# Kernel optimization log

Hardware: AMD Instinct MI355X
Metric: run time of the kernel (lower is better)

The kernel has to match this reference:

```python
import jax, jax.numpy as jnp
import numpy as np

K = 64        # num_clusters
S1 = 5        # num_shadow + 1
C = 128       # dim
ALPHA = 1500.0
EPS = 1e-12


def setup_inputs() -> dict:
    key = jax.random.key(0)
    k1, k2 = jax.random.split(key)
    x = jax.random.normal(k1, (8, C, 44, 44), dtype=jnp.float32)
    centroids = jax.random.normal(k2, (K, S1, C), dtype=jnp.float32) * 0.01
    return {"x": x, "centroids": centroids}


def reference(x, centroids):
    N = x.shape[0]
    # conv params derived from centroids, as in _init_params
    w = (2.0 * ALPHA) * centroids.reshape(K * S1, C)            # (K*S1, C)
    b = -ALPHA * jnp.linalg.norm(centroids.reshape(K * S1, C), axis=1)  # (K*S1,)

    xf = x.reshape(N, C, -1)                                    # (N, C, P)
    # 1x1 conv == GEMM over channel dim
    logits = jnp.einsum('mc,ncp->nmp', w, xf) + b[None, :, None]
    logits = logits.reshape(N, K, S1, -1)                       # (N, K, S1, P)

    soft_alpha = jax.nn.softmax(logits[:, :, 0:1, :], axis=1)   # (N, K, 1, P)
    soft_beta = jax.nn.softmax(logits, axis=2)[:, :, 0:1, :]    # (N, K, 1, P)
    soft_assign = soft_alpha * soft_beta                        # (N, K, 1, P)

    # residual = x - rep_centroid; then residual *= (1 + soft_assign); sum over P.
    # sum_p (x[n,c,p] - rep[k,c]) * w[n,k,p]
    #   = einsum(w, x) - rep[k,c] * sum_p w[n,k,p]   (same math, no (N,K,C,P) tensor)
    w_assign = 1.0 + soft_assign[:, :, 0, :]                    # (N, K, P)
    rep = centroids[:, 0, :]                                    # (K, C)
    out = jnp.einsum('nkp,ncp->nkc', w_assign, xf) \
          - rep[None, :, :] * jnp.sum(w_assign, axis=-1)[:, :, None]  # (N, K, C)

    # intra-cluster L2 normalize (dim=2), flatten, global L2 normalize
    out = out / jnp.maximum(jnp.linalg.norm(out, axis=2, keepdims=True), EPS)
    flat = out.reshape(N, -1)
    flat = flat / jnp.maximum(jnp.linalg.norm(flat, axis=1, keepdims=True), EPS)
    return (flat, soft_assign)
```

## Files before the change

kernel.cpp:

```cpp
#include <hip/hip_runtime.h>
#include <math.h>

#define NB 8
#define KC 64
#define S1C 5
#define CC 128
#define PP 1936
#define PT 64
#define NPT 31
#define NTILE (NB * NPT)
#define ALPHAF 1500.0f
#define EPSF 1e-12f

#define WS_PART  ((size_t)NTILE * KC * CC)
#define WS_MAIN_FLOATS (WS_PART + (size_t)NTILE * KC)

typedef __attribute__((ext_vector_type(8))) short short8;
typedef __attribute__((ext_vector_type(4))) float f32x4;

__device__ __forceinline__ void split8(const float4 a, const float4 b,
                                       short8& h, short8& l) {
    const float f[8] = {a.x, a.y, a.z, a.w, b.x, b.y, b.z, b.w};
#pragma unroll
    for (int j = 0; j < 8; ++j) {
        const unsigned u  = __float_as_uint(f[j]);
        const unsigned hi = u & 0xffff0000u;
        const float lo    = f[j] - __uint_as_float(hi);
        h[j] = (short)(hi >> 16);
        l[j] = (short)(__float_as_uint(lo) >> 16);
    }
}

__global__ __launch_bounds__(1024, 4) void k1_main(
    const float* __restrict__ x, const float* __restrict__ cen,
    float* __restrict__ sa_out, float* __restrict__ outC,
    float* __restrict__ outS, int mode)
{
    __shared__ __align__(16) unsigned short xh [64 * 128];
    __shared__ __align__(16) unsigned short xl [64 * 128];
    __shared__ __align__(16) unsigned short xch[128 * 64];
    __shared__ __align__(16) unsigned short xcl[128 * 64];
    __shared__ __align__(16) unsigned short wah[64 * 64];
    __shared__ __align__(16) unsigned short wal[64 * 64];
    __shared__ float2 ap[16 * 66];

    const int tid  = threadIdx.x;
    const int lane = tid & 63;
    const int wid  = tid >> 6;
    const int quad = lane >> 4;
    const int l15  = lane & 15;
    const int bx   = blockIdx.x;
    const int n    = bx / NPT;
    const int pt   = bx - n * NPT;
    const int p0   = pt * PT;

    int wrow[2]; bool wvalid[2];
#pragma unroll
    for (int i = 0; i < 2; ++i) {
        const int mp = (2 * wid + i) * 16 + l15;
        const int s  = mp & 7;
        wvalid[i] = (s < 5);
        wrow[i]   = 5 * (mp >> 3) + s;
    }

    float4 pv0[2], pv1[2];
#pragma unroll
    for (int i = 0; i < 2; ++i) {
        pv0[i] = make_float4(0.f, 0.f, 0.f, 0.f);
        pv1[i] = pv0[i];
        if (wvalid[i]) {
            const float* wp = cen + (size_t)wrow[i] * CC + quad * 8;
            pv0[i] = *(const float4*)wp;
            pv1[i] = *(const float4*)(wp + 4);
        }
    }

    const float* xn = x + (size_t)n * CC * PP;
    {
        const int pl = tid & 63;
        const int c0 = (tid >> 6) * 8;
        const bool pv = (p0 + pl) < PP;
        const float* src = xn + p0 + pl;
        float v[8];
#pragma unroll
        for (int i = 0; i < 8; ++i)
            v[i] = pv ? src[(size_t)(c0 + i) * PP] : 0.f;
        unsigned short hv[8], lv[8];
#pragma unroll
        for (int i = 0; i < 8; ++i) {
            const unsigned u  = __float_as_uint(v[i]);
            const unsigned hi = u & 0xffff0000u;
            hv[i] = (unsigned short)(hi >> 16);
            lv[i] = (unsigned short)(__float_as_uint(v[i] - __uint_as_float(hi)) >> 16);
        }
        short8 H8, L8;
#pragma unroll
        for (int i = 0; i < 8; ++i) { H8[i] = (short)hv[i]; L8[i] = (short)lv[i]; }
        const int sx = (pl * 128 + c0) ^ ((pl & 7) << 3);
        *(short8*)&xh[sx] = H8;
        *(short8*)&xl[sx] = L8;
#pragma unroll
        for (int i = 0; i < 8; ++i) {
            const int ci  = c0 + i;
            const int sc2 = (ci * 64 + pl) ^ ((ci & 7) << 3);
            xch[sc2] = hv[i];
            xcl[sc2] = lv[i];
        }
    }
    __syncthreads();

    f32x4 dacc[4][2];
#pragma unroll
    for (int a = 0; a < 4; ++a) {
        dacc[a][0] = (f32x4){0.f, 0.f, 0.f, 0.f};
        dacc[a][1] = (f32x4){0.f, 0.f, 0.f, 0.f};
    }
    float ssq[2] = {0.f, 0.f};

#pragma unroll 1
    for (int ks = 0; ks < 4; ++ks) {
        short8 ch[2], cl[2];
#pragma unroll
        for (int i = 0; i < 2; ++i) {
            const float4 a4 = pv0[i], b4 = pv1[i];
            ssq[i] += a4.x * a4.x + a4.y * a4.y + a4.z * a4.z + a4.w * a4.w
                    + b4.x * b4.x + b4.y * b4.y + b4.z * b4.z + b4.w * b4.w;
            split8(a4, b4, ch[i], cl[i]);
        }
        if (ks < 3) {
#pragma unroll
            for (int i = 0; i < 2; ++i) {
                pv0[i] = make_float4(0.f, 0.f, 0.f, 0.f);
                pv1[i] = pv0[i];
                if (wvalid[i]) {
                    const float* wp = cen + (size_t)wrow[i] * CC + (ks + 1) * 32 + quad * 8;
                    pv0[i] = *(const float4*)wp;
                    pv1[i] = *(const float4*)(wp + 4);
                }
            }
        }
#pragma unroll
        for (int a = 0; a < 4; ++a) {
            const int arow = a * 16 + l15;
            const int sidx = (arow * 128 + ks * 32 + quad * 8) ^ ((arow & 7) << 3);
            const short8 xh8 = *(const short8*)&xh[sidx];
            const short8 xl8 = *(const short8*)&xl[sidx];
#pragma unroll
            for (int i = 0; i < 2; ++i) {
                dacc[a][i] = __builtin_amdgcn_mfma_f32_16x16x32_bf16(ch[i], xh8, dacc[a][i], 0, 0, 0);
                dacc[a][i] = __builtin_amdgcn_mfma_f32_16x16x32_bf16(ch[i], xl8, dacc[a][i], 0, 0, 0);
                dacc[a][i] = __builtin_amdgcn_mfma_f32_16x16x32_bf16(cl[i], xh8, dacc[a][i], 0, 0, 0);
            }
        }
    }

    float bvr[2][4];
#pragma unroll
    for (int i = 0; i < 2; ++i) {
        float ss = ssq[i];
        ss += __shfl_xor(ss, 16);
        ss += __shfl_xor(ss, 32);
        const float bl = ((l15 & 7) < 5) ? (-ALPHAF * sqrtf(ss)) : -3.0e38f;
#pragma unroll
        for (int r = 0; r < 4; ++r)
            bvr[i][r] = __shfl(bl, quad * 4 + r);
    }

#pragma unroll
    for (int i = 0; i < 2; ++i)
#pragma unroll
        for (int a = 0; a < 4; ++a)
#pragma unroll
            for (int r = 0; r < 4; ++r)
                dacc[a][i][r] = 2.f * ALPHAF * dacc[a][i][r] + bvr[i][r];

#pragma unroll
    for (int a = 0; a < 4; ++a) {
        const float l0 = dacc[a][0][0];
        const float l1 = dacc[a][1][0];
        const float m2 = fmaxf(l0, l1);
        const float mo = __shfl_xor(m2, 32);
        const float m4 = fmaxf(m2, mo);
        float se = __expf(l0 - m4) + __expf(l1 - m4);
        se += __shfl_xor(se, 32);
        if ((lane & 48) == 0) ap[wid * 66 + a * 16 + l15] = make_float2(m4, se);
    }
    __syncthreads();

    float gmv, arv;
    {
        float gm = -3.0e38f;
#pragma unroll
        for (int w = 0; w < 16; ++w) gm = fmaxf(gm, ap[w * 66 + lane].x);
        float s = 0.f;
#pragma unroll
        for (int w = 0; w < 16; ++w) {
            const float2 v = ap[w * 66 + lane];
            s += v.y * __expf(v.x - gm);
        }
        gmv = gm; arv = 1.0f / s;
    }

    const int  kb  = 4 * wid + ((lane >> 5) & 1);
    const bool evq = ((lane & 16) == 0);
    float psum2[2] = {0.f, 0.f};
#pragma unroll
    for (int a = 0; a < 4; ++a) {
        const int p = a * 16 + l15;
        const float gm_p = __shfl(gmv, p);
        const float ar_p = __shfl(arv, p);
        const bool pvalid = (p0 + p) < PP;
#pragma unroll
        for (int i = 0; i < 2; ++i) {
            const f32x4 lg = dacc[a][i];
            const float s4 = __shfl_xor(lg[0], 16);
            float m5 = fmaxf(fmaxf(lg[0], lg[1]), fmaxf(lg[2], lg[3]));
            m5 = fmaxf(m5, s4);
            const float e0 = __expf(lg[0] - m5);
            const float d5 = e0 + __expf(lg[1] - m5) + __expf(lg[2] - m5)
                           + __expf(lg[3] - m5) + __expf(s4 - m5);
            const float sa = __expf(lg[0] - gm_p) * ar_p * (e0 / d5);
            const float wa = pvalid ? (1.0f + sa) : 0.0f;
            if (evq) {
                const int kk = kb + 2 * i;
                const int si = (kk * 64 + p) ^ ((kk & 7) << 3);
                const unsigned u  = __float_as_uint(wa);
                const unsigned hi = u & 0xffff0000u;
                wah[si] = (unsigned short)(hi >> 16);
                wal[si] = (unsigned short)(__float_as_uint(wa - __uint_as_float(hi)) >> 16);
            }
            psum2[i] += wa;
        }
    }
#pragma unroll
    for (int i = 0; i < 2; ++i) {
        float s = psum2[i];
        s += __shfl_xor(s, 1);
        s += __shfl_xor(s, 2);
        s += __shfl_xor(s, 4);
        s += __shfl_xor(s, 8);
        if ((lane & 31) == 0) {
            const int k = kb + 2 * i;
            if (mode == 0) outS[(size_t)bx * KC + k] = s;
            else           atomicAdd(&outS[(size_t)n * KC + k], s);
        }
    }
    __syncthreads();

    const int kt  = wid & 3;
    const int ct0 = (wid >> 2) * 2;
    f32x4 cacc[2];
    cacc[0] = (f32x4){0.f, 0.f, 0.f, 0.f};
    cacc[1] = (f32x4){0.f, 0.f, 0.f, 0.f};
#pragma unroll
    for (int ks = 0; ks < 64; ks += 32) {
        const int arow = kt * 16 + l15;
        const int sa_  = (arow * 64 + ks + quad * 8) ^ ((arow & 7) << 3);
        const short8 ah = *(const short8*)&wah[sa_];
        const short8 al = *(const short8*)&wal[sa_];
#pragma unroll
        for (int t = 0; t < 2; ++t) {
            const int crow = (ct0 + t) * 16 + l15;
            const int sb   = (crow * 64 + ks + quad * 8) ^ ((crow & 7) << 3);
            const short8 bh = *(const short8*)&xch[sb];
            const short8 bl = *(const short8*)&xcl[sb];
            cacc[t] = __builtin_amdgcn_mfma_f32_16x16x32_bf16(ah, bh, cacc[t], 0, 0, 0);
            cacc[t] = __builtin_amdgcn_mfma_f32_16x16x32_bf16(ah, bl, cacc[t], 0, 0, 0);
            cacc[t] = __builtin_amdgcn_mfma_f32_16x16x32_bf16(al, bh, cacc[t], 0, 0, 0);
        }
    }
    if (mode == 0) {
        float* dst = outC + (size_t)bx * KC * CC;
#pragma unroll
        for (int t = 0; t < 2; ++t) {
            const int c = (ct0 + t) * 16 + l15;
#pragma unroll
            for (int r = 0; r < 4; ++r)
                dst[(kt * 16 + 4 * quad + r) * CC + c] = cacc[t][r];
        }
    } else {
        float* dst = outC + (size_t)n * KC * CC;
#pragma unroll
        for (int t = 0; t < 2; ++t) {
            const int c = (ct0 + t) * 16 + l15;
#pragma unroll
            for (int r = 0; r < 4; ++r)
                atomicAdd(&dst[(kt * 16 + 4 * quad + r) * CC + c], cacc[t][r]);
        }
    }

    {
        float* san = sa_out + (size_t)n * KC * PP;
        const int k  = tid >> 4;
        const int p4 = (tid & 15) * 4;
        const int pg = p0 + p4;
        if (pg < PP) {
            const int si = (k * 64 + p4) ^ ((k & 7) << 3);
            const uint2 qh = *(const uint2*)&wah[si];
            const uint2 ql = *(const uint2*)&wal[si];
            const unsigned hh[2] = {qh.x, qh.y};
            const unsigned ll[2] = {ql.x, ql.y};
            float4 sv; float* svp = &sv.x;
#pragma unroll
            for (int j = 0; j < 4; ++j) {
                const unsigned h16 = (hh[j >> 1] >> ((j & 1) * 16)) & 0xffffu;
                const unsigned l16 = (ll[j >> 1] >> ((j & 1) * 16)) & 0xffffu;
                const float wa = __uint_as_float(h16 << 16) + __uint_as_float(l16 << 16);
                svp[j] = wa - 1.0f;
            }
            *(float4*)&san[(size_t)k * PP + pg] = sv;
        }
    }
}

__global__ __launch_bounds__(128) void k2_slab(
    const float* __restrict__ part, const float* __restrict__ ps,
    const float* __restrict__ cen, float* __restrict__ flat)
{
    __shared__ float w2[2];
    const int b = blockIdx.x;
    const int n = b >> 6;
    const int k = b & 63;
    const int c = threadIdx.x;
    const float* pb = part + (size_t)n * NPT * KC * CC + (size_t)k * CC + c;
    float v = 0.f;
#pragma unroll 8
    for (int pt = 0; pt < NPT; ++pt) v += pb[(size_t)pt * KC * CC];
    const float* psb = ps + (size_t)n * NPT * KC + k;
    float sw = 0.f;
#pragma unroll
    for (int pt = 0; pt < NPT; ++pt) sw += psb[(size_t)pt * KC];
    v -= cen[(size_t)k * S1C * CC + c] * sw;

    float ss = v * v;
#pragma unroll
    for (int off = 32; off > 0; off >>= 1) ss += __shfl_down(ss, off);
    if ((c & 63) == 0) w2[c >> 6] = ss;
    __syncthreads();
    const float norm = sqrtf(w2[0] + w2[1]);
    const float scale = 1.0f / (fmaxf(norm, EPSF) * 8.0f);
    flat[(size_t)b * CC + c] = v * scale;
}

__global__ __launch_bounds__(128) void k2_final(
    const float* __restrict__ accC, const float* __restrict__ accS,
    const float* __restrict__ cen, float* __restrict__ flat)
{
    __shared__ float w2[2];
    const int b = blockIdx.x;
    const int k = b & 63;
    const int c = threadIdx.x;
    const float v = accC[(size_t)b * CC + c] -
                    cen[(size_t)k * S1C * CC + c] * accS[b];
    float ss = v * v;
#pragma unroll
    for (int off = 32; off > 0; off >>= 1) ss += __shfl_down(ss, off);
    if ((c & 63) == 0) w2[c >> 6] = ss;
    __syncthreads();
    const float norm = sqrtf(w2[0] + w2[1]);
    const float scale = 1.0f / (fmaxf(norm, EPSF) * 8.0f);
    flat[(size_t)b * CC + c] = v * scale;
}

extern "C" void kernel_launch(void* const* d_in, const int* in_sizes, int n_in,
                              void* d_out, int out_size, void* d_ws, size_t ws_size,
                              hipStream_t stream) {
    const float* x   = (const float*)d_in[0];
    const float* cen = (const float*)d_in[1];
    float* out  = (float*)d_out;
    float* flat = out;
    float* sa   = out + (size_t)NB * KC * CC;
    float* ws   = (float*)d_ws;

    if (ws_size >= WS_MAIN_FLOATS * 4) {
        float* part = ws;
        float* ps   = part + WS_PART;
        k1_main<<<NTILE, 1024, 0, stream>>>(x, cen, sa, part, ps, 0);
        k2_slab<<<NB * KC, 128, 0, stream>>>(part, ps, cen, flat);
    } else {
        float* accC = ws;
        float* accS = accC + (size_t)NB * KC * CC;
        hipMemsetAsync(accC, 0, (size_t)(NB * KC * CC + NB * KC) * 4, stream);
        k1_main<<<NTILE, 1024, 0, stream>>>(x, cen, sa, accC, accS, 1);
        k2_final<<<NB * KC, 128, 0, stream>>>(accC, accS, cen, flat);
    }
}
```

Baseline: 80.37 us.

## Process two pixel tiles per block with both x tiles loaded upfront

Each 1024-thread block now handles two tiles, so the grid is halved (124 blocks instead of 248). Both x tiles are loaded and split into bf16 hi/lo shared buffers at the start, so the second tile's global load latency is covered by the first tile's compute. Shared memory use roughly doubles, and with only 124 blocks on a GPU with 256 CUs many CUs sit idle and per-block serial work doubles. The sa store was also moved before the second GEMM, which is safe because wah/wal are still intact at that point.

```diff
diff --git a/kernel.cpp b/kernel.cpp
--- a/kernel.cpp
+++ b/kernel.cpp
@@ -9,6 +9,7 @@
 #define PT 64
 #define NPT 31
 #define NTILE (NB * NPT)
+#define NBLK (NTILE / 2)
 #define ALPHAF 1500.0f
 #define EPSF 1e-12f
 
@@ -36,12 +37,16 @@
     float* __restrict__ sa_out, float* __restrict__ outC,
     float* __restrict__ outS, int mode)
 {
-    __shared__ __align__(16) unsigned short xh [64 * 128];
-    __shared__ __align__(16) unsigned short xl [64 * 128];
-    __shared__ __align__(16) unsigned short xch[128 * 64];
-    __shared__ __align__(16) unsigned short xcl[128 * 64];
-    __shared__ __align__(16) unsigned short wah[64 * 64];
-    __shared__ __align__(16) unsigned short wal[64 * 64];
+    __shared__ __align__(16) unsigned short xhA [64 * 128];
+    __shared__ __align__(16) unsigned short xlA [64 * 128];
+    __shared__ __align__(16) unsigned short xchA[128 * 64];
+    __shared__ __align__(16) unsigned short xclA[128 * 64];
+    __shared__ __align__(16) unsigned short xhB [64 * 128];
+    __shared__ __align__(16) unsigned short xlB [64 * 128];
+    __shared__ __align__(16) unsigned short xchB[128 * 64];
+    __shared__ __align__(16) unsigned short xclB[128 * 64];
+    __shared__ __align__(16) unsigned short wah [64 * 64];
+    __shared__ __align__(16) unsigned short wal [64 * 64];
     __shared__ float2 ap[16 * 66];
 
     const int tid  = threadIdx.x;
@@ -49,10 +54,8 @@
     const int wid  = tid >> 6;
     const int quad = lane >> 4;
     const int l15  = lane & 15;
-    const int bx   = blockIdx.x;
-    const int n    = bx / NPT;
-    const int pt   = bx - n * NPT;
-    const int p0   = pt * PT;
+    const int t1   = blockIdx.x;
+    const int t2   = blockIdx.x + NBLK;
 
     int wrow[2]; bool wvalid[2];
 #pragma unroll
@@ -63,254 +66,286 @@
         wrow[i]   = 5 * (mp >> 3) + s;
     }
 
-    float4 pv0[2], pv1[2];
+    float4 pv0i[2], pv1i[2];
 #pragma unroll
     for (int i = 0; i < 2; ++i) {
-        pv0[i] = make_float4(0.f, 0.f, 0.f, 0.f);
-        pv1[i] = pv0[i];
+        pv0i[i] = make_float4(0.f, 0.f, 0.f, 0.f);
+        pv1i[i] = pv0i[i];
         if (wvalid[i]) {
             const float* wp = cen + (size_t)wrow[i] * CC + quad * 8;
-            pv0[i] = *(const float4*)wp;
-            pv1[i] = *(const float4*)(wp + 4);
+            pv0i[i] = *(const float4*)wp;
+            pv1i[i] = *(const float4*)(wp + 4);
         }
     }
 
-    const float* xn = x + (size_t)n * CC * PP;
     {
         const int pl = tid & 63;
         const int c0 = (tid >> 6) * 8;
-        const bool pv = (p0 + pl) < PP;
-        const float* src = xn + p0 + pl;
-        float v[8];
-#pragma unroll
-        for (int i = 0; i < 8; ++i)
-            v[i] = pv ? src[(size_t)(c0 + i) * PP] : 0.f;
-        unsigned short hv[8], lv[8];
-#pragma unroll
-        for (int i = 0; i < 8; ++i) {
-            const unsigned u  = __float_as_uint(v[i]);
-            const unsigned hi = u & 0xffff0000u;
-            hv[i] = (unsigned short)(hi >> 16);
-            lv[i] = (unsigned short)(__float_as_uint(v[i] - __uint_as_float(hi)) >> 16);
-        }
-        short8 H8, L8;
-#pragma unroll
-        for (int i = 0; i < 8; ++i) { H8[i] = (short)hv[i]; L8[i] = (short)lv[i]; }
-        const int sx = (pl * 128 + c0) ^ ((pl & 7) << 3);
-        *(short8*)&xh[sx] = H8;
-        *(short8*)&xl[sx] = L8;
-#pragma unroll
-        for (int i = 0; i < 8; ++i) {
-            const int ci  = c0 + i;
-            const int sc2 = (ci * 64 + pl) ^ ((ci & 7) << 3);
-            xch[sc2] = hv[i];
-            xcl[sc2] = lv[i];
-        }
+        const int n1 = t1 / NPT, p01 = (t1 - n1 * NPT) * PT;
+        const int n2 = t2 / NPT, p02 = (t2 - n2 * NPT) * PT;
+        const bool pv1v = (p01 + pl) < PP;
+        const bool pv2v = (p02 + pl) < PP;
+        const float* s1 = x + (size_t)n1 * CC * PP + p01 + pl;
+        const float* s2 = x + (size_t)n2 * CC * PP + p02 + pl;
+        float v1[8], v2[8];
+#pragma unroll
+        for (int i = 0; i < 8; ++i) v1[i] = pv1v ? s1[(size_t)(c0 + i) * PP] : 0.f;
+#pragma unroll
+        for (int i = 0; i < 8; ++i) v2[i] = pv2v ? s2[(size_t)(c0 + i) * PP] : 0.f;
+
+        auto emit = [&](const float* v, unsigned short* xh_, unsigned short* xl_,
+                        unsigned short* xch_, unsigned short* xcl_) {
+            unsigned short hv[8], lv[8];
+#pragma unroll
+            for (int i = 0; i < 8; ++i) {
+                const unsigned u  = __float_as_uint(v[i]);
+                const unsigned hi = u & 0xffff0000u;
+                hv[i] = (unsigned short)(hi >> 16);
+                lv[i] = (unsigned short)(__float_as_uint(v[i] - __uint_as_float(hi)) >> 16);
+            }
+            short8 H8, L8;
+#pragma unroll
+            for (int i = 0; i < 8; ++i) { H8[i] = (short)hv[i]; L8[i] = (short)lv[i]; }
+            const int sx = (pl * 128 + c0) ^ ((pl & 7) << 3);
+            *(short8*)&xh_[sx] = H8;
+            *(short8*)&xl_[sx] = L8;
+#pragma unroll
+            for (int i = 0; i < 8; ++i) {
+                const int ci  = c0 + i;
+                const int sc2 = (ci * 64 + pl) ^ ((ci & 7) << 3);
+                xch_[sc2] = hv[i];
+                xcl_[sc2] = lv[i];
+            }
+        };
+        emit(v1, xhA, xlA, xchA, xclA);
+        emit(v2, xhB, xlB, xchB, xclB);
     }
     __syncthreads();
 
-    f32x4 dacc[4][2];
-#pragma unroll
-    for (int a = 0; a < 4; ++a) {
-        dacc[a][0] = (f32x4){0.f, 0.f, 0.f, 0.f};
-        dacc[a][1] = (f32x4){0.f, 0.f, 0.f, 0.f};
-    }
-    float ssq[2] = {0.f, 0.f};
+    auto do_tile = [&](const int t,
+                       const unsigned short* xh_, const unsigned short* xl_,
+                       const unsigned short* xch_, const unsigned short* xcl_) {
+        const int n  = t / NPT;
+        const int p0 = (t - n * NPT) * PT;
+
+        f32x4 dacc[4][2];
+#pragma unroll
+        for (int a = 0; a < 4; ++a) {
+            dacc[a][0] = (f32x4){0.f, 0.f, 0.f, 0.f};
+            dacc[a][1] = (f32x4){0.f, 0.f, 0.f, 0.f};
+        }
+        float ssq[2] = {0.f, 0.f};
+        float4 pv0[2], pv1[2];
+#pragma unroll
+        for (int i = 0; i < 2; ++i) { pv0[i] = pv0i[i]; pv1[i] = pv1i[i]; }
 
 #pragma unroll 1
-    for (int ks = 0; ks < 4; ++ks) {
-        short8 ch[2], cl[2];
+        for (int ks = 0; ks < 4; ++ks) {
+            short8 ch[2], cl[2];
+#pragma unroll
+            for (int i = 0; i < 2; ++i) {
+                const float4 a4 = pv0[i], b4 = pv1[i];
+                ssq[i] += a4.x * a4.x + a4.y * a4.y + a4.z * a4.z + a4.w * a4.w
+                        + b4.x * b4.x + b4.y * b4.y + b4.z * b4.z + b4.w * b4.w;
+                split8(a4, b4, ch[i], cl[i]);
+            }
+            if (ks < 3) {
+#pragma unroll
+                for (int i = 0; i < 2; ++i) {
+                    pv0[i] = make_float4(0.f, 0.f, 0.f, 0.f);
+                    pv1[i] = pv0[i];
+                    if (wvalid[i]) {
+                        const float* wp = cen + (size_t)wrow[i] * CC + (ks + 1) * 32 + quad * 8;
+                        pv0[i] = *(const float4*)wp;
+                        pv1[i] = *(const float4*)(wp + 4);
+                    }
+                }
+            }
+#pragma unroll
+            for (int a = 0; a < 4; ++a) {
+                const int arow = a * 16 + l15;
+                const int sidx = (arow * 128 + ks * 32 + quad * 8) ^ ((arow & 7) << 3);
+                const short8 xh8 = *(const short8*)&xh_[sidx];
+                const short8 xl8 = *(const short8*)&xl_[sidx];
+#pragma unroll
+                for (int i = 0; i < 2; ++i) {
+                    dacc[a][i] = __builtin_amdgcn_mfma_f32_16x16x32_bf16(ch[i], xh8, dacc[a][i], 0, 0, 0);
+                    dacc[a][i] = __builtin_amdgcn_mfma_f32_16x16x32_bf16(ch[i], xl8, dacc[a][i], 0, 0, 0);
+                    dacc[a][i] = __builtin_amdgcn_mfma_f32_16x16x32_bf16(cl[i], xh8, dacc[a][i], 0, 0, 0);
+                }
+            }
+        }
+
 #pragma unroll
         for (int i = 0; i < 2; ++i) {
-            const float4 a4 = pv0[i], b4 = pv1[i];
-            ssq[i] += a4.x * a4.x + a4.y * a4.y + a4.z * a4.z + a4.w * a4.w
-                    + b4.x * b4.x + b4.y * b4.y + b4.z * b4.z + b4.w * b4.w;
-            split8(a4, b4, ch[i], cl[i]);
-        }
-        if (ks < 3) {
+            if (wvalid[i]) {
+                const float* wp = cen + (size_t)wrow[i] * CC + quad * 8;
+                pv0i[i] = *(const float4*)wp;
+                pv1i[i] = *(const float4*)(wp + 4);
+            }
+        }
+
+        float bvr[2][4];
+#pragma unroll
+        for (int i = 0; i < 2; ++i) {
+            float ss = ssq[i];
+            ss += __shfl_xor(ss, 16);
+            ss += __shfl_xor(ss, 32);
+            const float bl = ((l15 & 7) < 5) ? (-ALPHAF * sqrtf(ss)) : -3.0e38f;
+#pragma unroll
+            for (int r = 0; r < 4; ++r)
+                bvr[i][r] = __shfl(bl, quad * 4 + r);
+        }
+#pragma unroll
+        for (int i = 0; i < 2; ++i)
+#pragma unroll
+            for (int a = 0; a < 4; ++a)
+#pragma unroll
+                for (int r = 0; r < 4; ++r)
+                    dacc[a][i][r] = 2.f * ALPHAF * dacc[a][i][r] + bvr[i][r];
+
+#pragma unroll
+        for (int a = 0; a < 4; ++a) {
+            const float l0 = dacc[a][0][0];
+            const float l1 = dacc[a][1][0];
+            const float m2 = fmaxf(l0, l1);
+            const float mo = __shfl_xor(m2, 32);
+            const float m4 = fmaxf(m2, mo);
+            float se = __expf(l0 - m4) + __expf(l1 - m4);
+            se += __shfl_xor(se, 32);
+            if ((lane & 48) == 0) ap[wid * 66 + a * 16 + l15] = make_float2(m4, se);
+        }
+        __syncthreads();
+
+        float gmv, arv;
+        {
+            float gm = -3.0e38f;
+#pragma unroll
+            for (int w = 0; w < 16; ++w) gm = fmaxf(gm, ap[w * 66 + lane].x);
+            float s = 0.f;
+#pragma unroll
+            for (int w = 0; w < 16; ++w) {
+                const float2 v = ap[w * 66 + lane];
+                s += v.y * __expf(v.x - gm);
+            }
+            gmv = gm; arv = 1.0f / s;
+        }
+
+        const int  kb  = 4 * wid + ((lane >> 5) & 1);
+        const bool evq = ((lane & 16) == 0);
+        float psum2[2] = {0.f, 0.f};
+#pragma unroll
+        for (int a = 0; a < 4; ++a) {
+            const int p = a * 16 + l15;
+            const float gm_p = __shfl(gmv, p);
+            const float ar_p = __shfl(arv, p);
+            const bool pvalid = (p0 + p) < PP;
 #pragma unroll
             for (int i = 0; i < 2; ++i) {
-                pv0[i] = make_float4(0.f, 0.f, 0.f, 0.f);
-                pv1[i] = pv0[i];
-                if (wvalid[i]) {
-                    const float* wp = cen + (size_t)wrow[i] * CC + (ks + 1) * 32 + quad * 8;
-                    pv0[i] = *(const float4*)wp;
-                    pv1[i] = *(const float4*)(wp + 4);
+                const f32x4 lg = dacc[a][i];
+                const float s4 = __shfl_xor(lg[0], 16);
+                float m5 = fmaxf(fmaxf(lg[0], lg[1]), fmaxf(lg[2], lg[3]));
+                m5 = fmaxf(m5, s4);
+                const float e0 = __expf(lg[0] - m5);
+                const float d5 = e0 + __expf(lg[1] - m5) + __expf(lg[2] - m5)
+                               + __expf(lg[3] - m5) + __expf(s4 - m5);
+                const float sa = __expf(lg[0] - gm_p) * ar_p * (e0 / d5);
+                const float wa = pvalid ? (1.0f + sa) : 0.0f;
+                if (evq) {
+                    const int kk = kb + 2 * i;
+                    const int si = (kk * 64 + p) ^ ((kk & 7) << 3);
+                    const unsigned u  = __float_as_uint(wa);
+                    const unsigned hi = u & 0xffff0000u;
+                    wah[si] = (unsigned short)(hi >> 16);
+                    wal[si] = (unsigned short)(__float_as_uint(wa - __uint_as_float(hi)) >> 16);
                 }
-            }
-        }
-#pragma unroll
-        for (int a = 0; a < 4; ++a) {
-            const int arow = a * 16 + l15;
-            const int sidx = (arow * 128 + ks * 32 + quad * 8) ^ ((arow & 7) << 3);
-            const short8 xh8 = *(const short8*)&xh[sidx];
-            const short8 xl8 = *(const short8*)&xl[sidx];
-#pragma unroll
-            for (int i = 0; i < 2; ++i) {
-                dacc[a][i] = __builtin_amdgcn_mfma_f32_16x16x32_bf16(ch[i], xh8, dacc[a][i], 0, 0, 0);
-                dacc[a][i] = __builtin_amdgcn_mfma_f32_16x16x32_bf16(ch[i], xl8, dacc[a][i], 0, 0, 0);
-                dacc[a][i] = __builtin_amdgcn_mfma_f32_16x16x32_bf16(cl[i], xh8, dacc[a][i], 0, 0, 0);
-            }
-        }
-    }
-
-    float bvr[2][4];
-#pragma unroll
-    for (int i = 0; i < 2; ++i) {
-        float ss = ssq[i];
-        ss += __shfl_xor(ss, 16);
-        ss += __shfl_xor(ss, 32);
-        const float bl = ((l15 & 7) < 5) ? (-ALPHAF * sqrtf(ss)) : -3.0e38f;
-#pragma unroll
-        for (int r = 0; r < 4; ++r)
-            bvr[i][r] = __shfl(bl, quad * 4 + r);
-    }
-
-#pragma unroll
-    for (int i = 0; i < 2; ++i)
-#pragma unroll
-        for (int a = 0; a < 4; ++a)
-#pragma unroll
-            for (int r = 0; r < 4; ++r)
-                dacc[a][i][r] = 2.f * ALPHAF * dacc[a][i][r] + bvr[i][r];
-
-#pragma unroll
-    for (int a = 0; a < 4; ++a) {
-        const float l0 = dacc[a][0][0];
-        const float l1 = dacc[a][1][0];
-        const float m2 = fmaxf(l0, l1);
-        const float mo = __shfl_xor(m2, 32);
-        const float m4 = fmaxf(m2, mo);
-        float se = __expf(l0 - m4) + __expf(l1 - m4);
-        se += __shfl_xor(se, 32);
-        if ((lane & 48) == 0) ap[wid * 66 + a * 16 + l15] = make_float2(m4, se);
-    }
+                psum2[i] += wa;
+            }
+        }
+#pragma unroll
+        for (int i = 0; i < 2; ++i) {
+            float s = psum2[i];
+            s += __shfl_xor(s, 1);
+            s += __shfl_xor(s, 2);
+            s += __shfl_xor(s, 4);
+            s += __shfl_xor(s, 8);
+            if ((lane & 31) == 0) {
+                const int k = kb + 2 * i;
+                if (mode == 0) outS[(size_t)t * KC + k] = s;
+                else           atomicAdd(&outS[(size_t)n * KC + k], s);
+            }
+        }
+        __syncthreads();
+
+        {
+            float* san = sa_out + (size_t)n * KC * PP;
+            const int k  = tid >> 4;
+            const int p4 = (tid & 15) * 4;
+            const int pg = p0 + p4;
+            if (pg < PP) {
+                const int si = (k * 64 + p4) ^ ((k & 7) << 3);
+                const uint2 qh = *(const uint2*)&wah[si];
+                const uint2 ql = *(const uint2*)&wal[si];
+                const unsigned hh[2] = {qh.x, qh.y};
+                const unsigned ll[2] = {ql.x, ql.y};
+                float4 sv; float* svp = &sv.x;
+#pragma unroll
+                for (int j = 0; j < 4; ++j) {
+                    const unsigned h16 = (hh[j >> 1] >> ((j & 1) * 16)) & 0xffffu;
+                    const unsigned l16 = (ll[j >> 1] >> ((j & 1) * 16)) & 0xffffu;
+                    const float wa = __uint_as_float(h16 << 16) + __uint_as_float(l16 << 16);
+                    svp[j] = wa - 1.0f;
+                }
+                *(float4*)&san[(size_t)k * PP + pg] = sv;
+            }
+        }
+
+        const int kt  = wid & 3;
+        const int ct0 = (wid >> 2) * 2;
+        f32x4 cacc[2];
+        cacc[0] = (f32x4){0.f, 0.f, 0.f, 0.f};
+        cacc[1] = (f32x4){0.f, 0.f, 0.f, 0.f};
+#pragma unroll
+        for (int ks = 0; ks < 64; ks += 32) {
+            const int arow = kt * 16 + l15;
+            const int sa_  = (arow * 64 + ks + quad * 8) ^ ((arow & 7) << 3);
+            const short8 ah = *(const short8*)&wah[sa_];
+            const short8 al = *(const short8*)&wal[sa_];
+#pragma unroll
+            for (int tt = 0; tt < 2; ++tt) {
+                const int crow = (ct0 + tt) * 16 + l15;
+                const int sb   = (crow * 64 + ks + quad * 8) ^ ((crow & 7) << 3);
+                const short8 bh = *(const short8*)&xch_[sb];
+                const short8 bl = *(const short8*)&xcl_[sb];
+                cacc[tt] = __builtin_amdgcn_mfma_f32_16x16x32_bf16(ah, bh, cacc[tt], 0, 0, 0);
+                cacc[tt] = __builtin_amdgcn_mfma_f32_16x16x32_bf16(ah, bl, cacc[tt], 0, 0, 0);
+                cacc[tt] = __builtin_amdgcn_mfma_f32_16x16x32_bf16(al, bh, cacc[tt], 0, 0, 0);
+            }
+        }
+        if (mode == 0) {
+            float* dst = outC + (size_t)t * KC * CC;
+#pragma unroll
+            for (int tt = 0; tt < 2; ++tt) {
+                const int c = (ct0 + tt) * 16 + l15;
+#pragma unroll
+                for (int r = 0; r < 4; ++r)
+                    dst[(kt * 16 + 4 * quad + r) * CC + c] = cacc[tt][r];
+            }
+        } else {
+            float* dst = outC + (size_t)n * KC * CC;
+#pragma unroll
+            for (int tt = 0; tt < 2; ++tt) {
+                const int c = (ct0 + tt) * 16 + l15;
+#pragma unroll
+                for (int r = 0; r < 4; ++r)
+                    atomicAdd(&dst[(kt * 16 + 4 * quad + r) * CC + c], cacc[tt][r]);
+            }
+        }
+    };
+
+    do_tile(t1, xhA, xlA, xchA, xclA);
     __syncthreads();
-
-    float gmv, arv;
-    {
-        float gm = -3.0e38f;
-#pragma unroll
-        for (int w = 0; w < 16; ++w) gm = fmaxf(gm, ap[w * 66 + lane].x);
-        float s = 0.f;
-#pragma unroll
-        for (int w = 0; w < 16; ++w) {
-            const float2 v = ap[w * 66 + lane];
-            s += v.y * __expf(v.x - gm);
-        }
-        gmv = gm; arv = 1.0f / s;
-    }
-
-    const int  kb  = 4 * wid + ((lane >> 5) & 1);
-    const bool evq = ((lane & 16) == 0);
-    float psum2[2] = {0.f, 0.f};
-#pragma unroll
-    for (int a = 0; a < 4; ++a) {
-        const int p = a * 16 + l15;
-        const float gm_p = __shfl(gmv, p);
-        const float ar_p = __shfl(arv, p);
-        const bool pvalid = (p0 + p) < PP;
-#pragma unroll
-        for (int i = 0; i < 2; ++i) {
-            const f32x4 lg = dacc[a][i];
-            const float s4 = __shfl_xor(lg[0], 16);
-            float m5 = fmaxf(fmaxf(lg[0], lg[1]), fmaxf(lg[2], lg[3]));
-            m5 = fmaxf(m5, s4);
-            const float e0 = __expf(lg[0] - m5);
-            const float d5 = e0 + __expf(lg[1] - m5) + __expf(lg[2] - m5)
-                           + __expf(lg[3] - m5) + __expf(s4 - m5);
-            const float sa = __expf(lg[0] - gm_p) * ar_p * (e0 / d5);
-            const float wa = pvalid ? (1.0f + sa) : 0.0f;
-            if (evq) {
-                const int kk = kb + 2 * i;
-                const int si = (kk * 64 + p) ^ ((kk & 7) << 3);
-                const unsigned u  = __float_as_uint(wa);
-                const unsigned hi = u & 0xffff0000u;
-                wah[si] = (unsigned short)(hi >> 16);
-                wal[si] = (unsigned short)(__float_as_uint(wa - __uint_as_float(hi)) >> 16);
-            }
-            psum2[i] += wa;
-        }
-    }
-#pragma unroll
-    for (int i = 0; i < 2; ++i) {
-        float s = psum2[i];
-        s += __shfl_xor(s, 1);
-        s += __shfl_xor(s, 2);
-        s += __shfl_xor(s, 4);
-        s += __shfl_xor(s, 8);
-        if ((lane & 31) == 0) {
-            const int k = kb + 2 * i;
-            if (mode == 0) outS[(size_t)bx * KC + k] = s;
-            else           atomicAdd(&outS[(size_t)n * KC + k], s);
-        }
-    }
-    __syncthreads();
-
-    const int kt  = wid & 3;
-    const int ct0 = (wid >> 2) * 2;
-    f32x4 cacc[2];
-    cacc[0] = (f32x4){0.f, 0.f, 0.f, 0.f};
-    cacc[1] = (f32x4){0.f, 0.f, 0.f, 0.f};
-#pragma unroll
-    for (int ks = 0; ks < 64; ks += 32) {
-        const int arow = kt * 16 + l15;
-        const int sa_  = (arow * 64 + ks + quad * 8) ^ ((arow & 7) << 3);
-        const short8 ah = *(const short8*)&wah[sa_];
-        const short8 al = *(const short8*)&wal[sa_];
-#pragma unroll
-        for (int t = 0; t < 2; ++t) {
-            const int crow = (ct0 + t) * 16 + l15;
-            const int sb   = (crow * 64 + ks + quad * 8) ^ ((crow & 7) << 3);
-            const short8 bh = *(const short8*)&xch[sb];
-            const short8 bl = *(const short8*)&xcl[sb];
-            cacc[t] = __builtin_amdgcn_mfma_f32_16x16x32_bf16(ah, bh, cacc[t], 0, 0, 0);
-            cacc[t] = __builtin_amdgcn_mfma_f32_16x16x32_bf16(ah, bl, cacc[t], 0, 0, 0);
-            cacc[t] = __builtin_amdgcn_mfma_f32_16x16x32_bf16(al, bh, cacc[t], 0, 0, 0);
-        }
-    }
-    if (mode == 0) {
-        float* dst = outC + (size_t)bx * KC * CC;
-#pragma unroll
-        for (int t = 0; t < 2; ++t) {
-            const int c = (ct0 + t) * 16 + l15;
-#pragma unroll
-            for (int r = 0; r < 4; ++r)
-                dst[(kt * 16 + 4 * quad + r) * CC + c] = cacc[t][r];
-        }
-    } else {
-        float* dst = outC + (size_t)n * KC * CC;
-#pragma unroll
-        for (int t = 0; t < 2; ++t) {
-            const int c = (ct0 + t) * 16 + l15;
-#pragma unroll
-            for (int r = 0; r < 4; ++r)
-                atomicAdd(&dst[(kt * 16 + 4 * quad + r) * CC + c], cacc[t][r]);
-        }
-    }
-
-    {
-        float* san = sa_out + (size_t)n * KC * PP;
-        const int k  = tid >> 4;
-        const int p4 = (tid & 15) * 4;
-        const int pg = p0 + p4;
-        if (pg < PP) {
-            const int si = (k * 64 + p4) ^ ((k & 7) << 3);
-            const uint2 qh = *(const uint2*)&wah[si];
-            const uint2 ql = *(const uint2*)&wal[si];
-            const unsigned hh[2] = {qh.x, qh.y};
-            const unsigned ll[2] = {ql.x, ql.y};
-            float4 sv; float* svp = &sv.x;
-#pragma unroll
-            for (int j = 0; j < 4; ++j) {
-                const unsigned h16 = (hh[j >> 1] >> ((j & 1) * 16)) & 0xffffu;
-                const unsigned l16 = (ll[j >> 1] >> ((j & 1) * 16)) & 0xffffu;
-                const float wa = __uint_as_float(h16 << 16) + __uint_as_float(l16 << 16);
-                svp[j] = wa - 1.0f;
-            }
-            *(float4*)&san[(size_t)k * PP + pg] = sv;
-        }
-    }
+    do_tile(t2, xhB, xlB, xchB, xclB);
 }
 
 __global__ __launch_bounds__(128) void k2_slab(
@@ -375,13 +410,13 @@
     if (ws_size >= WS_MAIN_FLOATS * 4) {
         float* part = ws;
         float* ps   = part + WS_PART;
-        k1_main<<<NTILE, 1024, 0, stream>>>(x, cen, sa, part, ps, 0);
+        k1_main<<<NBLK, 1024, 0, stream>>>(x, cen, sa, part, ps, 0);
         k2_slab<<<NB * KC, 128, 0, stream>>>(part, ps, cen, flat);
     } else {
         float* accC = ws;
         float* accS = accC + (size_t)NB * KC * CC;
         hipMemsetAsync(accC, 0, (size_t)(NB * KC * CC + NB * KC) * 4, stream);
-        k1_main<<<NTILE, 1024, 0, stream>>>(x, cen, sa, accC, accS, 1);
+        k1_main<<<NBLK, 1024, 0, stream>>>(x, cen, sa, accC, accS, 1);
         k2_final<<<NB * KC, 128, 0, stream>>>(accC, accS, cen, flat);
     }
 }
```

Result: slower. 91.82 us (+14.2%).
